# Kernel optimization log

Hardware: AMD Instinct MI355X
Metric: run time of the kernel (lower is better)

The kernel has to match this reference:

```python
import jax, jax.numpy as jnp
import numpy as np

EPS = 1e-5

def _ln(z, g, b):
    # LayerNorm over last axis (per the gammas/betas of shape (2, 3H))
    mu = jnp.mean(z, axis=-1, keepdims=True)
    var = jnp.var(z, axis=-1, keepdims=True)
    return g * (z - mu) * jax.lax.rsqrt(var + EPS) + b

def setup_inputs() -> dict:
    key = jax.random.key(0)
    ks = jax.random.split(key, 12)
    B, L, D_IN, H, A, DEPTH = 64, 512, 256, 256, 128, 4
    glorot = lambda k, sh: jax.random.normal(k, sh, jnp.float32) * np.sqrt(2.0 / (sh[0] + sh[1])).astype(np.float32)
    # variable-length prefix masks (bucketing/masking semantics of the layer)
    lengths = jax.random.randint(ks[0], (B, 1), L // 2, L + 1)
    mask = jnp.arange(L)[None, :] < lengths
    return {
        'x': jax.random.normal(ks[1], (B, L, D_IN), jnp.float32),
        'mask': mask,
        'W_emb': glorot(ks[2], (D_IN, H)),
        'b_emb': jnp.zeros((H,), jnp.float32),
        'W': glorot(ks[3], (H, 3 * H)),
        'U': glorot(ks[4], (H, 3 * H)),
        'b': jnp.zeros((3 * H,), jnp.float32),
        'W_action_1': glorot(ks[5], (H, A)),
        'U_action_1': glorot(ks[6], (H, A)),
        'b_action_1': jnp.zeros((A,), jnp.float32),
        'W_action_2': glorot(ks[7], (A, 2)),
        'b_action_2': jnp.zeros((2,), jnp.float32),
        'gammas': jnp.ones((2, 3 * H), jnp.float32),
        'betas': jnp.zeros((2, 3 * H), jnp.float32),
        'depth': DEPTH,
    }

def _run_depth(x_seq, m_seq, W, U, b, Wa1, Ua1, ba1, Wa2, ba2, gammas, betas):
    # x_seq: (L,B,H), m_seq: (L,B) bool
    H = W.shape[0]
    B = x_seq.shape[1]
    # precompute + layernorm the input projection for all steps (fusable)
    xp_all = _ln(jnp.einsum('lbh,hk->lbk', x_seq, W), gammas[0], betas[0])  # (L,B,3H)

    def step(h, inputs):
        xp, xt, mt = inputs  # (B,3H), (B,H), (B,)
        hp = _ln(h @ U, gammas[1], betas[1])
        r = jax.nn.sigmoid(xp[:, :H] + hp[:, :H] + b[:H])
        z = jax.nn.sigmoid(xp[:, H:2 * H] + hp[:, H:2 * H] + b[H:2 * H])
        hh = jnp.tanh(xp[:, 2 * H:] + r * hp[:, 2 * H:] + b[2 * H:])
        h_new = z * h + (1.0 - z) * hh
        # action-policy subnetwork (binary merge/propagate decision)
        logits = jnp.tanh(xt @ Wa1 + h @ Ua1 + ba1) @ Wa2 + ba2  # (B,2)
        pol = jax.nn.softmax(logits, axis=-1)
        act = (pol[:, 1] > pol[:, 0]) & mt
        h_out = jnp.where(mt[:, None], h_new, h)  # masked steps carry state
        return h_out, (h_out, act, pol)

    h0 = jnp.zeros((B, H), x_seq.dtype)
    _, (h_seq, act_seq, pol_seq) = jax.lax.scan(step, h0, (xp_all, x_seq, m_seq))
    return h_seq, act_seq, pol_seq

def reference(x, mask, W_emb, b_emb, W, U, b, W_action_1, U_action_1, b_action_1,
              W_action_2, b_action_2, gammas, betas, depth):
    # embedding projection, then time-major like the Theano scans
    h_seq = jnp.swapaxes(x @ W_emb + b_emb, 0, 1)  # (L,B,H)
    m_seq = jnp.swapaxes(mask, 0, 1)               # (L,B)
    actions, policies = [], []
    for _ in range(depth):  # vertical (tree-depth) scan: small fixed count
        h_new, act, pol = _run_depth(h_seq, m_seq, W, U, b,
                                     W_action_1, U_action_1, b_action_1,
                                     W_action_2, b_action_2, gammas, betas)
        actions.append(act)
        policies.append(pol)
        h_seq = h_new
        m_seq = m_seq & act  # tree collapse: only selected nodes survive upward
    output = h_seq[-1]  # (B,H) final hidden state of top layer
    action = jnp.stack(actions, 0).transpose(2, 0, 1)      # (B,depth,L)
    policy = jnp.stack(policies, 0).transpose(2, 0, 1, 3)  # (B,depth,L,2)
    return output, action, policy
```

## Files before the change

kernel.cpp:

```cpp
#include <hip/hip_runtime.h>
#include <hip/hip_bf16.h>
#include <math.h>

#define BB 64
#define LL 512
#define HH 256
#define H3 768
#define AA 128
#define NDEPTH 4
#define NROWS (LL*BB)

#define EXCH_U64_PER_CHAIN (2 * 3 * 256)

typedef float vf32x32 __attribute__((ext_vector_type(32)));

__global__ void maskcvt_kernel(const unsigned char* __restrict__ raw,
                               int* __restrict__ m)
{
    int i = blockIdx.x * blockDim.x + threadIdx.x;
    bool bytemode = (raw[1] == 1);
    int v;
    if (bytemode) v = raw[i] ? 1 : 0;
    else          v = (((const int*)raw)[i] != 0) ? 1 : 0;
    m[i] = v;
}

__global__ __launch_bounds__(512) void mkidx_kernel(
    const int* __restrict__ m,
    int* __restrict__ rowidx,
    int* __restrict__ nact)
{
    const int b    = blockIdx.x;
    const int tid  = threadIdx.x;
    const int lane = tid & 63;
    const int w    = tid >> 6;
    __shared__ int wcnt[8];
    int pred = m[b * LL + tid];
    unsigned long long bal = __ballot(pred != 0);
    int below = __popcll(bal & ((1ull << lane) - 1ull));
    if (lane == 63) wcnt[w] = __popcll(bal);
    __syncthreads();
    int woff = 0;
#pragma unroll
    for (int i = 0; i < 8; ++i) woff += (i < w) ? wcnt[i] : 0;
    if (pred) rowidx[b * LL + woff + below] = tid;
    if (tid == 511) nact[b] = woff + wcnt[7];
}

template<int MODE, int EPI>
__global__ __launch_bounds__(256) void gemm_kernel(
    const float* __restrict__ A, const float* __restrict__ Bm,
    const float* __restrict__ bias,
    float* __restrict__ C, int M, int N,
    const int* __restrict__ ridx, const int* __restrict__ nact)
{
    __shared__ float As[16][132];
    __shared__ float Bs[16][132];
    const int tid = threadIdx.x;
    const int tx = tid & 15, ty = tid >> 4;
    const int row0 = blockIdx.y * 128, col0 = blockIdx.x * 128;

    int arow0 = 0, arow1 = 0;
    if (MODE == 3) {
        const int bb = row0 >> 9;
        const int na = nact[bb];
        if ((row0 & 511) >= na) return;
        const int r0 = row0 + (tid >> 2);
        const int r1 = r0 + 64;
        const int l0 = ((r0 & 511) < na) ? ridx[r0] : 0;
        const int l1 = ((r1 & 511) < na) ? ridx[r1] : 0;
        arow0 = l0 * 64 + bb;
        arow1 = l1 * 64 + bb;
    }

    float acc[8][8];
#pragma unroll
    for (int i = 0; i < 8; ++i)
#pragma unroll
        for (int j = 0; j < 8; ++j) acc[i][j] = 0.f;

    for (int kk = 0; kk < 256; kk += 16) {
#pragma unroll
        for (int i = 0; i < 2; ++i) {
            int aid = i * 256 + tid;
            int r   = aid >> 2;
            int k4  = (aid & 3) << 2;
            int rr  = row0 + r;
            float4 v;
            if (MODE == 1) {
                v = *(const float4*)(A + (rr & 63) * 131072 + (rr >> 6) * 256 + kk + k4);
            } else {
                int ar = i ? arow1 : arow0;
                v = *(const float4*)(A + ar * 256 + kk + k4);
            }
            As[k4 + 0][r] = v.x; As[k4 + 1][r] = v.y;
            As[k4 + 2][r] = v.z; As[k4 + 3][r] = v.w;

            int bid = i * 256 + tid;
            int bk  = bid >> 5;
            int c4  = (bid & 31) << 2;
            float4 w = *(const float4*)(Bm + (kk + bk) * N + col0 + c4);
            *(float4*)&Bs[bk][c4] = w;
        }
        __syncthreads();
#pragma unroll
        for (int k = 0; k < 16; ++k) {
            float a[8], bb2[8];
            *(float4*)&a[0]   = *(const float4*)&As[k][ty * 8];
            *(float4*)&a[4]   = *(const float4*)&As[k][ty * 8 + 4];
            *(float4*)&bb2[0] = *(const float4*)&Bs[k][tx * 8];
            *(float4*)&bb2[4] = *(const float4*)&Bs[k][tx * 8 + 4];
#pragma unroll
            for (int i = 0; i < 8; ++i)
#pragma unroll
                for (int j = 0; j < 8; ++j)
                    acc[i][j] += a[i] * bb2[j];
        }
        __syncthreads();
    }

#pragma unroll
    for (int i = 0; i < 8; ++i) {
        int row  = row0 + ty * 8 + i;
        int colb = col0 + tx * 8;
        float vout[8];
#pragma unroll
        for (int j = 0; j < 8; ++j) {
            float v = acc[i][j];
            if (EPI == 1) v += bias[colb + j];
            vout[j] = v;
        }
        *(float4*)&C[row * N + colb]     = *(float4*)&vout[0];
        *(float4*)&C[row * N + colb + 4] = *(float4*)&vout[4];
    }
}

__global__ __launch_bounds__(256) void lnrows_kernel(
    float* __restrict__ XP, const float* __restrict__ g0,
    const float* __restrict__ b0, const float* __restrict__ gb,
    const int* __restrict__ nact)
{
    const int row = blockIdx.x;
    if ((row & 511) >= nact[row >> 9]) return;
    const int tid = threadIdx.x;
    float* p = XP + (long)row * H3;
    float v0 = p[tid], v1 = p[tid + 256], v2 = p[tid + 512];
    float s = v0 + v1 + v2;
    float q = v0 * v0 + v1 * v1 + v2 * v2;
#pragma unroll
    for (int off = 32; off >= 1; off >>= 1) {
        s += __shfl_xor(s, off);
        q += __shfl_xor(q, off);
    }
    __shared__ float rs4[4], rq4[4];
    if ((tid & 63) == 0) { rs4[tid >> 6] = s; rq4[tid >> 6] = q; }
    __syncthreads();
    float S = rs4[0] + rs4[1] + rs4[2] + rs4[3];
    float Q = rq4[0] + rq4[1] + rq4[2] + rq4[3];
    float mu  = S * (1.f / 768.f);
    float var = Q * (1.f / 768.f) - mu * mu;
    float r   = rsqrtf(var + 1e-5f);
    p[tid]       = g0[tid]       * (v0 - mu) * r + b0[tid]       + gb[tid];
    p[tid + 256] = g0[tid + 256] * (v1 - mu) * r + b0[tid + 256] + gb[tid + 256];
    p[tid + 512] = g0[tid + 512] * (v2 - mu) * r + b0[tid + 512] + gb[tid + 512];
}

__global__ __launch_bounds__(512, 2) void scan3_kernel(
    const float* __restrict__ XP,
    const float* __restrict__ U,
    const float* __restrict__ g1, const float* __restrict__ b1,
    const int* __restrict__ mask,
    float* __restrict__ Y,
    unsigned long long* __restrict__ exch,
    int seq0,
    const float* __restrict__ Xc,
    const float* __restrict__ Wa1,
    const float* __restrict__ ba1,
    float* __restrict__ XA)
{
    __shared__ float h_cur[256];
    __shared__ float part[16][256];
    __shared__ float xp_lds[768];
    __shared__ float g1s[768], b1s[768];
    __shared__ int   mk[512];
    __shared__ float reds[4], redq[4];
    __shared__ float As[16][132];
    __shared__ float Bs[16][132];

    const int tid = threadIdx.x;

    if (blockIdx.x >= 192) {
        const int t    = blockIdx.x - 192;
        const int row0 = t * 128;
        const int tx   = tid & 15;
        const int ty4  = tid >> 4;
        float xacc[4][8];
#pragma unroll
        for (int i = 0; i < 4; ++i)
#pragma unroll
            for (int j = 0; j < 8; ++j) xacc[i][j] = 0.f;

        for (int kk = 0; kk < 256; kk += 16) {
            {
                int r  = tid >> 2;
                int k4 = (tid & 3) << 2;
                float4 v = *(const float4*)(Xc + (row0 + r) * 256 + kk + k4);
                As[k4 + 0][r] = v.x; As[k4 + 1][r] = v.y;
                As[k4 + 2][r] = v.z; As[k4 + 3][r] = v.w;
            }
            {
                int bk = tid >> 5;
                int c4 = (tid & 31) << 2;
                float4 w = *(const float4*)(Wa1 + (kk + bk) * AA + c4);
                *(float4*)&Bs[bk][c4] = w;
            }
            __syncthreads();
#pragma unroll
            for (int k = 0; k < 16; ++k) {
                float a[4], bb2[8];
                *(float4*)&a[0]   = *(const float4*)&As[k][ty4 * 4];
                *(float4*)&bb2[0] = *(const float4*)&Bs[k][tx * 8];
                *(float4*)&bb2[4] = *(const float4*)&Bs[k][tx * 8 + 4];
#pragma unroll
                for (int i = 0; i < 4; ++i)
#pragma unroll
                    for (int j = 0; j < 8; ++j)
                        xacc[i][j] += a[i] * bb2[j];
            }
            __syncthreads();
        }
#pragma unroll
        for (int i = 0; i < 4; ++i) {
            int row  = row0 + ty4 * 4 + i;
            int colb = tx * 8;
            float vout[8];
#pragma unroll
            for (int j = 0; j < 8; ++j) vout[j] = xacc[i][j] + ba1[colb + j];
            *(float4*)&XA[row * AA + colb]     = *(float4*)&vout[0];
            *(float4*)&XA[row * AA + colb + 4] = *(float4*)&vout[4];
        }
        return;
    }

    const int i0   = blockIdx.x;
    const int xcd  = i0 & 7;
    const int slot = i0 >> 3;
    const int b    = xcd + 8 * (slot / 3);
    const int s    = slot % 3;
    const int kg   = tid >> 5;
    const int cg   = tid & 31;
    const int q1   = (s + 1 >= 3) ? s - 2 : s + 1;
    const int q2   = (s + 2 >= 3) ? s - 1 : s + 2;

    vf32x32 u0v, u1v, u2v, u3v;
    {
        const volatile float* Uv = U;
        const int colbase = s * 256 + cg;
#pragma unroll
        for (int i = 0; i < 16; ++i) {
#pragma unroll
            for (int j = 0; j < 8; ++j) {
                const int f = i * 8 + j;
                float val = Uv[(kg * 16 + i) * H3 + colbase + 32 * j];
                if      (f < 32) u0v[f]      = val;
                else if (f < 64) u1v[f - 32] = val;
                else if (f < 96) u2v[f - 64] = val;
                else             u3v[f - 96] = val;
            }
        }
    }
    if (tid < 256) h_cur[tid] = 0.f;
    for (int i = tid; i < 768; i += 512) { g1s[i] = g1[i]; b1s[i] = b1[i]; }
    mk[tid] = mask[b * LL + tid];
    __syncthreads();

    unsigned long long* exb = exch + b * EXCH_U64_PER_CHAIN;
    int seq = seq0;

    for (int l = 0; l < LL; ++l) {
        if (!mk[l]) {
            if (s == 0 && tid < 64) {
                float4 hv = *(const float4*)&h_cur[tid * 4];
                *(float4*)&Y[((long)l * BB + b) * HH + tid * 4] = hv;
            }
            continue;
        }
        seq++;
        const int par = seq & 1;
        const int cs  = seq - seq0 - 1;

        float4 xr4;
        if (tid < 192) xr4 = *(const float4*)(XP + ((long)(b * LL + cs)) * H3 + tid * 4);

        float acc[8] = {0.f, 0.f, 0.f, 0.f, 0.f, 0.f, 0.f, 0.f};
#pragma unroll
        for (int i = 0; i < 4; ++i) {
            float4 hv = *(const float4*)&h_cur[kg * 16 + i * 4];
#pragma unroll
            for (int e = 0; e < 4; ++e) {
                const float hh = (e == 0) ? hv.x : (e == 1) ? hv.y
                               : (e == 2) ? hv.z : hv.w;
                const int ik = i * 4 + e;
#pragma unroll
                for (int j = 0; j < 8; ++j) {
                    const int f = ik * 8 + j;
                    const float uu = (f < 32) ? u0v[f]
                                   : (f < 64) ? u1v[f - 32]
                                   : (f < 96) ? u2v[f - 64]
                                   :            u3v[f - 96];
                    acc[j] += uu * hh;
                }
            }
        }
#pragma unroll
        for (int j = 0; j < 8; ++j)
            part[kg][cg + 32 * j] = acc[j];
        __syncthreads();

        if (tid < 192) *(float4*)&xp_lds[tid * 4] = xr4;

        float pre = 0.f, v0 = 0.f, v1 = 0.f, v2 = 0.f;
        if (tid < 256) {
            pre = part[0][tid];
#pragma unroll
            for (int gg = 1; gg < 16; ++gg) pre += part[gg][tid];

            unsigned long long pk =
                ((unsigned long long)(unsigned)seq << 32) |
                (unsigned long long)__float_as_uint(pre);
            __hip_atomic_store(&exb[(par * 3 + s) * 256 + tid], pk,
                               __ATOMIC_RELAXED, __HIP_MEMORY_SCOPE_AGENT);

            unsigned long long x1 = 0, x2 = 0;
            bool d1 = false, d2 = false;
            int spins = 0;
            do {
                unsigned long long t1 =
                    __hip_atomic_load(&exb[(par * 3 + q1) * 256 + tid],
                                      __ATOMIC_RELAXED, __HIP_MEMORY_SCOPE_AGENT);
                unsigned long long t2 =
                    __hip_atomic_load(&exb[(par * 3 + q2) * 256 + tid],
                                      __ATOMIC_RELAXED, __HIP_MEMORY_SCOPE_AGENT);
                if (!d1 && (int)(t1 >> 32) == seq) { x1 = t1; d1 = true; }
                if (!d2 && (int)(t2 >> 32) == seq) { x2 = t2; d2 = true; }
                if (++spins > 8) __builtin_amdgcn_s_sleep(1);
            } while (!(d1 && d2));
            float w1 = __uint_as_float((unsigned)x1);
            float w2 = __uint_as_float((unsigned)x2);
            v0 = (s == 0) ? pre : ((q1 == 0) ? w1 : w2);
            v1 = (s == 1) ? pre : ((q1 == 1) ? w1 : w2);
            v2 = (s == 2) ? pre : ((q1 == 2) ? w1 : w2);

            float st = v0 + v1 + v2;
            float qt = v0 * v0 + v1 * v1 + v2 * v2;
#pragma unroll
            for (int off = 32; off >= 1; off >>= 1) {
                st += __shfl_xor(st, off);
                qt += __shfl_xor(qt, off);
            }
            if ((tid & 63) == 0) { reds[tid >> 6] = st; redq[tid >> 6] = qt; }
        }
        __syncthreads();

        if (tid < 256) {
            float S = reds[0] + reds[1] + reds[2] + reds[3];
            float Q = redq[0] + redq[1] + redq[2] + redq[3];
            float mu = S * (1.f / 768.f);
            float rs = rsqrtf(Q * (1.f / 768.f) - mu * mu + 1e-5f);
            float hp_r = g1s[tid]       * (v0 - mu) * rs + b1s[tid];
            float hp_z = g1s[256 + tid] * (v1 - mu) * rs + b1s[256 + tid];
            float hp_h = g1s[512 + tid] * (v2 - mu) * rs + b1s[512 + tid];
            float xr = xp_lds[tid], xz = xp_lds[256 + tid], xh = xp_lds[512 + tid];
            float r  = 1.f / (1.f + expf(-(xr + hp_r)));
            float z  = 1.f / (1.f + expf(-(xz + hp_z)));
            float hh = tanhf(xh + r * hp_h);
            float o  = z * h_cur[tid] + (1.f - z) * hh;
            h_cur[tid] = o;
            if (s == 0) Y[((long)l * BB + b) * HH + tid] = o;
        }
        __syncthreads();
    }
}

__global__ __launch_bounds__(256) void gemmact_kernel(
    const float* __restrict__ Yprev,
    const float* __restrict__ Ua1,
    const float* __restrict__ XA,
    const float* __restrict__ Wa2,
    const float* __restrict__ ba2,
    const int* __restrict__ mask_in, int* __restrict__ mask_out,
    float* __restrict__ act_out, float* __restrict__ pol_out, int d)
{
    __shared__ float As[16][132];
    __shared__ float Bs[16][132];
    const int tid = threadIdx.x;
    const int tx = tid & 15, ty = tid >> 4;
    const int row0 = blockIdx.y * 128;

    float acc[8][8];
#pragma unroll
    for (int i = 0; i < 8; ++i)
#pragma unroll
        for (int j = 0; j < 8; ++j) acc[i][j] = 0.f;

    for (int kk = 0; kk < 256; kk += 16) {
#pragma unroll
        for (int i = 0; i < 2; ++i) {
            int aid = i * 256 + tid;
            int r   = aid >> 2;
            int k4  = (aid & 3) << 2;
            int rr  = row0 + r;
            float4 v;
            if (rr < 64) v = make_float4(0.f, 0.f, 0.f, 0.f);
            else         v = *(const float4*)(Yprev + (rr - 64) * 256 + kk + k4);
            As[k4 + 0][r] = v.x; As[k4 + 1][r] = v.y;
            As[k4 + 2][r] = v.z; As[k4 + 3][r] = v.w;

            int bid = i * 256 + tid;
            int bk  = bid >> 5;
            int c4  = (bid & 31) << 2;
            float4 w = *(const float4*)(Ua1 + (kk + bk) * AA + c4);
            *(float4*)&Bs[bk][c4] = w;
        }
        __syncthreads();
#pragma unroll
        for (int k = 0; k < 16; ++k) {
            float a[8], bb2[8];
            *(float4*)&a[0]   = *(const float4*)&As[k][ty * 8];
            *(float4*)&a[4]   = *(const float4*)&As[k][ty * 8 + 4];
            *(float4*)&bb2[0] = *(const float4*)&Bs[k][tx * 8];
            *(float4*)&bb2[4] = *(const float4*)&Bs[k][tx * 8 + 4];
#pragma unroll
            for (int i = 0; i < 8; ++i)
#pragma unroll
                for (int j = 0; j < 8; ++j)
                    acc[i][j] += a[i] * bb2[j];
        }
        __syncthreads();
    }

    float p0[8], p1[8];
#pragma unroll
    for (int i = 0; i < 8; ++i) { p0[i] = 0.f; p1[i] = 0.f; }
#pragma unroll
    for (int i = 0; i < 8; ++i) {
        int row  = row0 + ty * 8 + i;
#pragma unroll
        for (int j = 0; j < 8; ++j) {
            int c   = tx * 8 + j;
            float v = tanhf(acc[i][j] + XA[row * AA + c]);
            p0[i] += v * Wa2[c * 2];
            p1[i] += v * Wa2[c * 2 + 1];
        }
    }
#pragma unroll
    for (int off = 1; off < 16; off <<= 1) {
#pragma unroll
        for (int i = 0; i < 8; ++i) {
            p0[i] += __shfl_xor(p0[i], off);
            p1[i] += __shfl_xor(p1[i], off);
        }
    }
    if (tx == 0) {
#pragma unroll
        for (int i = 0; i < 8; ++i) {
            int row = row0 + ty * 8 + i;
            int l   = row >> 6, bb = row & 63;
            float l0 = p0[i] + ba2[0];
            float l1 = p1[i] + ba2[1];
            float m  = fmaxf(l0, l1);
            float e0 = expf(l0 - m), e1 = expf(l1 - m);
            float inv = 1.f / (e0 + e1);
            float q0 = e0 * inv, q1v = e1 * inv;
            int mt = mask_in[bb * LL + l];
            int a  = (q1v > q0) && mt;
            act_out[bb * (NDEPTH * LL) + d * LL + l] = a ? 1.f : 0.f;
            pol_out[bb * (NDEPTH * LL * 2) + d * (LL * 2) + l * 2 + 0] = q0;
            pol_out[bb * (NDEPTH * LL * 2) + d * (LL * 2) + l * 2 + 1] = q1v;
            mask_out[bb * LL + l] = a;
        }
    }
}

__global__ void final_copy_kernel(const float* __restrict__ X, float* __restrict__ out)
{
    int i = blockIdx.x * blockDim.x + threadIdx.x;
    int bb = i >> 8, j = i & 255;
    out[i] = X[((long)(LL - 1) * BB + bb) * HH + j];
}

extern "C" void kernel_launch(void* const* d_in, const int* in_sizes, int n_in,
                              void* d_out, int out_size, void* d_ws, size_t ws_size,
                              hipStream_t stream)
{
    const float* x      = (const float*)d_in[0];
    const void*  mraw   = d_in[1];
    const float* W_emb  = (const float*)d_in[2];
    const float* b_emb  = (const float*)d_in[3];
    const float* W      = (const float*)d_in[4];
    const float* U      = (const float*)d_in[5];
    const float* bias3  = (const float*)d_in[6];
    const float* Wa1    = (const float*)d_in[7];
    const float* Ua1    = (const float*)d_in[8];
    const float* ba1    = (const float*)d_in[9];
    const float* Wa2    = (const float*)d_in[10];
    const float* ba2    = (const float*)d_in[11];
    const float* gammas = (const float*)d_in[12];
    const float* betas  = (const float*)d_in[13];

    float* out = (float*)d_out;
    char*  ws  = (char*)d_ws;

    float* XP = (float*)(ws);
    float* X  = (float*)(ws + 100663296UL);
    float* Y  = (float*)(ws + 134217728UL);
    float* XA = (float*)(ws + 167772160UL);
    int*   m0 = (int*)(ws + 184549376UL);
    int*   m1 = (int*)(ws + 184680448UL);
    unsigned long long* exch_d = (unsigned long long*)(ws + 184811520UL);

    float* act_out = out + BB * HH;
    float* pol_out = act_out + BB * NDEPTH * LL;

    maskcvt_kernel<<<dim3(NROWS / 256), dim3(256), 0, stream>>>(
        (const unsigned char*)mraw, m0);

    gemm_kernel<1, 1><<<dim3(2, 256), dim3(256), 0, stream>>>(
        x, W_emb, b_emb, X, NROWS, HH, nullptr, nullptr);

    float* Xc = X; float* Yc = Y;
    int* mc = m0; int* mn = m1;

    for (int d = 0; d < NDEPTH; ++d) {
        int* rowidx = (int*)Yc;
        int* nactp  = ((int*)Yc) + NROWS;

        mkidx_kernel<<<dim3(BB), dim3(512), 0, stream>>>(mc, rowidx, nactp);

        gemm_kernel<3, 0><<<dim3(6, 256), dim3(256), 0, stream>>>(
            Xc, W, nullptr, XP, NROWS, H3, rowidx, nactp);
        lnrows_kernel<<<dim3(NROWS), dim3(256), 0, stream>>>(
            XP, gammas, betas, bias3, nactp);

        scan3_kernel<<<dim3(448), dim3(512), 0, stream>>>(
            XP, U, gammas + H3, betas + H3, mc, Yc, exch_d, d << 10,
            Xc, Wa1, ba1, XA);

        gemmact_kernel<<<dim3(1, 256), dim3(256), 0, stream>>>(
            Yc, Ua1, XA, Wa2, ba2, mc, mn, act_out, pol_out, d);

        { float* tmp = Xc; Xc = Yc; Yc = tmp; }
        { int* tmp = mc; mc = mn; mn = tmp; }
    }

    final_copy_kernel<<<dim3(BB), dim3(256), 0, stream>>>(Xc, out);
}
```

Measured before the change: 3.263 ms.

## Remap scan matvec to shuffle-reduced columns and fix LDS bank conflicts in GEMMs

The recurrent h@U matvec in the scan kernel now gives each thread 4 adjacent output columns over a 32-row k-slice. Partial sums are reduced with warp shuffles across 8 lanes, which replaces the 16x256 shared-memory partial array and its serial 16-way sum. The hidden state is kept in a padded LDS layout to avoid bank conflicts, and the exchange stores are issued straight from the reducing lanes. The tiled GEMMs change their B-fragment column mapping from tx*8 to split tx*4 / 64+tx*4 to reduce LDS bank conflicts, with matching epilogue indexing.

```diff
diff --git a/kernel.cpp b/kernel.cpp
--- a/kernel.cpp
+++ b/kernel.cpp
@@ -13,6 +13,12 @@
 #define EXCH_U64_PER_CHAIN (2 * 3 * 256)
 
 typedef float vf32x32 __attribute__((ext_vector_type(32)));
+
+#define HIDX(c) (36 * ((c) >> 5) + ((c) & 31))
+#define HPAD 284
+
+#define UVAL(f) ((f) < 32 ? u0v[(f)] : (f) < 64 ? u1v[(f)-32] \
+                : (f) < 96 ? u2v[(f)-64] : u3v[(f)-96])
 
 __global__ void maskcvt_kernel(const unsigned char* __restrict__ raw,
                                int* __restrict__ m)
@@ -108,8 +114,8 @@
             float a[8], bb2[8];
             *(float4*)&a[0]   = *(const float4*)&As[k][ty * 8];
             *(float4*)&a[4]   = *(const float4*)&As[k][ty * 8 + 4];
-            *(float4*)&bb2[0] = *(const float4*)&Bs[k][tx * 8];
-            *(float4*)&bb2[4] = *(const float4*)&Bs[k][tx * 8 + 4];
+            *(float4*)&bb2[0] = *(const float4*)&Bs[k][tx * 4];
+            *(float4*)&bb2[4] = *(const float4*)&Bs[k][64 + tx * 4];
 #pragma unroll
             for (int i = 0; i < 8; ++i)
 #pragma unroll
@@ -121,17 +127,18 @@
 
 #pragma unroll
     for (int i = 0; i < 8; ++i) {
-        int row  = row0 + ty * 8 + i;
-        int colb = col0 + tx * 8;
-        float vout[8];
-#pragma unroll
-        for (int j = 0; j < 8; ++j) {
-            float v = acc[i][j];
-            if (EPI == 1) v += bias[colb + j];
-            vout[j] = v;
-        }
-        *(float4*)&C[row * N + colb]     = *(float4*)&vout[0];
-        *(float4*)&C[row * N + colb + 4] = *(float4*)&vout[4];
+        int row   = row0 + ty * 8 + i;
+        int colb0 = col0 + tx * 4;
+        int colb1 = col0 + 64 + tx * 4;
+        float v0[4], v1[4];
+#pragma unroll
+        for (int j = 0; j < 4; ++j) {
+            float a0 = acc[i][j], a1 = acc[i][4 + j];
+            if (EPI == 1) { a0 += bias[colb0 + j]; a1 += bias[colb1 + j]; }
+            v0[j] = a0; v1[j] = a1;
+        }
+        *(float4*)&C[row * N + colb0] = *(float4*)&v0[0];
+        *(float4*)&C[row * N + colb1] = *(float4*)&v1[0];
     }
 }
 
@@ -178,8 +185,8 @@
     const float* __restrict__ ba1,
     float* __restrict__ XA)
 {
-    __shared__ float h_cur[256];
-    __shared__ float part[16][256];
+    __shared__ float h_pad[HPAD];
+    __shared__ float vrow[256];
     __shared__ float xp_lds[768];
     __shared__ float g1s[768], b1s[768];
     __shared__ int   mk[512];
@@ -219,8 +226,8 @@
             for (int k = 0; k < 16; ++k) {
                 float a[4], bb2[8];
                 *(float4*)&a[0]   = *(const float4*)&As[k][ty4 * 4];
-                *(float4*)&bb2[0] = *(const float4*)&Bs[k][tx * 8];
-                *(float4*)&bb2[4] = *(const float4*)&Bs[k][tx * 8 + 4];
+                *(float4*)&bb2[0] = *(const float4*)&Bs[k][tx * 4];
+                *(float4*)&bb2[4] = *(const float4*)&Bs[k][64 + tx * 4];
 #pragma unroll
                 for (int i = 0; i < 4; ++i)
 #pragma unroll
@@ -231,13 +238,15 @@
         }
 #pragma unroll
         for (int i = 0; i < 4; ++i) {
-            int row  = row0 + ty4 * 4 + i;
-            int colb = tx * 8;
-            float vout[8];
-#pragma unroll
-            for (int j = 0; j < 8; ++j) vout[j] = xacc[i][j] + ba1[colb + j];
-            *(float4*)&XA[row * AA + colb]     = *(float4*)&vout[0];
-            *(float4*)&XA[row * AA + colb + 4] = *(float4*)&vout[4];
+            int row = row0 + ty4 * 4 + i;
+            float v0[4], v1[4];
+#pragma unroll
+            for (int j = 0; j < 4; ++j) {
+                v0[j] = xacc[i][j]     + ba1[tx * 4 + j];
+                v1[j] = xacc[i][4 + j] + ba1[64 + tx * 4 + j];
+            }
+            *(float4*)&XA[row * AA + tx * 4]      = *(float4*)&v0[0];
+            *(float4*)&XA[row * AA + 64 + tx * 4] = *(float4*)&v1[0];
         }
         return;
     }
@@ -247,21 +256,22 @@
     const int slot = i0 >> 3;
     const int b    = xcd + 8 * (slot / 3);
     const int s    = slot % 3;
-    const int kg   = tid >> 5;
-    const int cg   = tid & 31;
+    const int kg   = tid & 7;
+    const int cp   = tid >> 3;
     const int q1   = (s + 1 >= 3) ? s - 2 : s + 1;
     const int q2   = (s + 2 >= 3) ? s - 1 : s + 2;
 
     vf32x32 u0v, u1v, u2v, u3v;
     {
         const volatile float* Uv = U;
-        const int colbase = s * 256 + cg;
-#pragma unroll
-        for (int i = 0; i < 16; ++i) {
-#pragma unroll
-            for (int j = 0; j < 8; ++j) {
-                const int f = i * 8 + j;
-                float val = Uv[(kg * 16 + i) * H3 + colbase + 32 * j];
+        const int colbase = s * 256 + 4 * cp;
+#pragma unroll
+        for (int i = 0; i < 8; ++i) {
+#pragma unroll
+            for (int t = 0; t < 16; ++t) {
+                const int e = t >> 2, cj = t & 3;
+                const int f = i * 16 + t;
+                float val = Uv[(32 * kg + 4 * i + e) * H3 + colbase + cj];
                 if      (f < 32) u0v[f]      = val;
                 else if (f < 64) u1v[f - 32] = val;
                 else if (f < 96) u2v[f - 64] = val;
@@ -269,7 +279,7 @@
             }
         }
     }
-    if (tid < 256) h_cur[tid] = 0.f;
+    for (int i = tid; i < HPAD; i += 512) h_pad[i] = 0.f;
     for (int i = tid; i < 768; i += 512) { g1s[i] = g1[i]; b1s[i] = b1[i]; }
     mk[tid] = mask[b * LL + tid];
     __syncthreads();
@@ -280,7 +290,7 @@
     for (int l = 0; l < LL; ++l) {
         if (!mk[l]) {
             if (s == 0 && tid < 64) {
-                float4 hv = *(const float4*)&h_cur[tid * 4];
+                float4 hv = *(const float4*)&h_pad[HIDX(tid * 4)];
                 *(float4*)&Y[((long)l * BB + b) * HH + tid * 4] = hv;
             }
             continue;
@@ -292,44 +302,57 @@
         float4 xr4;
         if (tid < 192) xr4 = *(const float4*)(XP + ((long)(b * LL + cs)) * H3 + tid * 4);
 
-        float acc[8] = {0.f, 0.f, 0.f, 0.f, 0.f, 0.f, 0.f, 0.f};
-#pragma unroll
-        for (int i = 0; i < 4; ++i) {
-            float4 hv = *(const float4*)&h_cur[kg * 16 + i * 4];
+        float a0 = 0.f, a1 = 0.f, a2 = 0.f, a3 = 0.f;
+#pragma unroll
+        for (int i = 0; i < 8; ++i) {
+            const float4 hv = *(const float4*)&h_pad[36 * kg + 4 * i];
 #pragma unroll
             for (int e = 0; e < 4; ++e) {
                 const float hh = (e == 0) ? hv.x : (e == 1) ? hv.y
                                : (e == 2) ? hv.z : hv.w;
-                const int ik = i * 4 + e;
-#pragma unroll
-                for (int j = 0; j < 8; ++j) {
-                    const int f = ik * 8 + j;
-                    const float uu = (f < 32) ? u0v[f]
-                                   : (f < 64) ? u1v[f - 32]
-                                   : (f < 96) ? u2v[f - 64]
-                                   :            u3v[f - 96];
-                    acc[j] += uu * hh;
-                }
-            }
-        }
-#pragma unroll
-        for (int j = 0; j < 8; ++j)
-            part[kg][cg + 32 * j] = acc[j];
+                const int fb = i * 16 + e * 4;
+                a0 += UVAL(fb + 0) * hh;
+                a1 += UVAL(fb + 1) * hh;
+                a2 += UVAL(fb + 2) * hh;
+                a3 += UVAL(fb + 3) * hh;
+            }
+        }
+#pragma unroll
+        for (int off = 1; off < 8; off <<= 1) {
+            a0 += __shfl_xor(a0, off);
+            a1 += __shfl_xor(a1, off);
+            a2 += __shfl_xor(a2, off);
+            a3 += __shfl_xor(a3, off);
+        }
+
+        if (kg < 2) {
+            const int c0 = 4 * cp + 2 * kg;
+            const float pv0 = (kg == 0) ? a0 : a2;
+            const float pv1 = (kg == 0) ? a1 : a3;
+            unsigned long long pk0 =
+                ((unsigned long long)(unsigned)seq << 32) |
+                (unsigned long long)__float_as_uint(pv0);
+            unsigned long long pk1 =
+                ((unsigned long long)(unsigned)seq << 32) |
+                (unsigned long long)__float_as_uint(pv1);
+            __hip_atomic_store(&exb[(par * 3 + s) * 256 + c0], pk0,
+                               __ATOMIC_RELAXED, __HIP_MEMORY_SCOPE_AGENT);
+            __hip_atomic_store(&exb[(par * 3 + s) * 256 + c0 + 1], pk1,
+                               __ATOMIC_RELAXED, __HIP_MEMORY_SCOPE_AGENT);
+        } else if (kg == 2) {
+            vrow[4 * cp]     = a0;
+            vrow[4 * cp + 1] = a1;
+        } else if (kg == 3) {
+            vrow[4 * cp + 2] = a2;
+            vrow[4 * cp + 3] = a3;
+        }
         __syncthreads();
 
         if (tid < 192) *(float4*)&xp_lds[tid * 4] = xr4;
 
         float pre = 0.f, v0 = 0.f, v1 = 0.f, v2 = 0.f;
         if (tid < 256) {
-            pre = part[0][tid];
-#pragma unroll
-            for (int gg = 1; gg < 16; ++gg) pre += part[gg][tid];
-
-            unsigned long long pk =
-                ((unsigned long long)(unsigned)seq << 32) |
-                (unsigned long long)__float_as_uint(pre);
-            __hip_atomic_store(&exb[(par * 3 + s) * 256 + tid], pk,
-                               __ATOMIC_RELAXED, __HIP_MEMORY_SCOPE_AGENT);
+            pre = vrow[tid];
 
             unsigned long long x1 = 0, x2 = 0;
             bool d1 = false, d2 = false;
@@ -374,8 +397,8 @@
             float r  = 1.f / (1.f + expf(-(xr + hp_r)));
             float z  = 1.f / (1.f + expf(-(xz + hp_z)));
             float hh = tanhf(xh + r * hp_h);
-            float o  = z * h_cur[tid] + (1.f - z) * hh;
-            h_cur[tid] = o;
+            float o  = z * h_pad[HIDX(tid)] + (1.f - z) * hh;
+            h_pad[HIDX(tid)] = o;
             if (s == 0) Y[((long)l * BB + b) * HH + tid] = o;
         }
         __syncthreads();
@@ -428,8 +451,8 @@
             float a[8], bb2[8];
             *(float4*)&a[0]   = *(const float4*)&As[k][ty * 8];
             *(float4*)&a[4]   = *(const float4*)&As[k][ty * 8 + 4];
-            *(float4*)&bb2[0] = *(const float4*)&Bs[k][tx * 8];
-            *(float4*)&bb2[4] = *(const float4*)&Bs[k][tx * 8 + 4];
+            *(float4*)&bb2[0] = *(const float4*)&Bs[k][tx * 4];
+            *(float4*)&bb2[4] = *(const float4*)&Bs[k][64 + tx * 4];
 #pragma unroll
             for (int i = 0; i < 8; ++i)
 #pragma unroll
@@ -444,10 +467,10 @@
     for (int i = 0; i < 8; ++i) { p0[i] = 0.f; p1[i] = 0.f; }
 #pragma unroll
     for (int i = 0; i < 8; ++i) {
-        int row  = row0 + ty * 8 + i;
+        int row = row0 + ty * 8 + i;
 #pragma unroll
         for (int j = 0; j < 8; ++j) {
-            int c   = tx * 8 + j;
+            int c   = (j < 4) ? (tx * 4 + j) : (64 + tx * 4 + (j - 4));
             float v = tanhf(acc[i][j] + XA[row * AA + c]);
             p0[i] += v * Wa2[c * 2];
             p1[i] += v * Wa2[c * 2 + 1];
```

After: 3.275 ms. No clear change (+0.4%).
